# Optimization experiments

Hardware: AMD Instinct MI355X
Metric: run time of the kernel (lower is better)

The kernel has to match this reference:

```python
import jax, jax.numpy as jnp
import numpy as np

N = 50000      # nodes
E = 800000     # edges (before self loops)
IN_DIM = 256
HID = 64       # per-head hidden dim
HEADS = 4
NEG_SLOPE = 0.2


def setup_inputs() -> dict:
    key = jax.random.key(0)
    k1, k2, k3, k4, k5, k6 = jax.random.split(key, 6)
    x = jax.random.normal(k1, (N, IN_DIM), dtype=jnp.float32)
    edge_index = jax.random.randint(k2, (2, E), 0, N, dtype=jnp.int64)
    # GATConv params (PyG layout): lin weight, att_src, att_dst, bias
    W = jax.random.normal(k3, (IN_DIM, HEADS * HID), dtype=jnp.float32) / np.sqrt(IN_DIM)
    att_src = jax.random.normal(k4, (HEADS, HID), dtype=jnp.float32) / np.sqrt(HID)
    att_dst = jax.random.normal(k5, (HEADS, HID), dtype=jnp.float32) / np.sqrt(HID)
    bias = jnp.zeros((HEADS * HID,), dtype=jnp.float32)
    return {"x": x, "edge_index": edge_index, "W": W,
            "att_src": att_src, "att_dst": att_dst, "bias": bias}


def _gat_forward(x, edge_index, W, att_src, att_dst, bias):
    n = x.shape[0]
    # linear projection per head: [N, H, F]
    h = (x @ W).reshape(n, HEADS, HID)
    # per-node attention logits (computed once on nodes, then gathered)
    a_src = jnp.einsum('nhf,hf->nh', h, att_src)  # [N, H]
    a_dst = jnp.einsum('nhf,hf->nh', h, att_dst)  # [N, H]
    # add self loops (PyG default add_self_loops=True)
    loop = jnp.arange(n, dtype=edge_index.dtype)
    src = jnp.concatenate([edge_index[0], loop])  # [E+N]
    dst = jnp.concatenate([edge_index[1], loop])  # [E+N]
    # edge attention logits with LeakyReLU
    e = jax.nn.leaky_relu(a_src[src] + a_dst[dst], NEG_SLOPE)  # [E+N, H]
    # segment softmax over incoming edges of each destination node
    m = jax.ops.segment_max(e, dst, num_segments=n)            # [N, H]
    num = jnp.exp(e - m[dst])                                  # [E+N, H]
    denom = jax.ops.segment_sum(num, dst, num_segments=n)      # [N, H]
    alpha = num / denom[dst]                                   # [E+N, H]
    # scatter-aggregate weighted source features
    msg = alpha[:, :, None] * h[src]                           # [E+N, H, F]
    out = jax.ops.segment_sum(msg, dst, num_segments=n)        # [N, H, F]
    out = out.reshape(n, HEADS * HID) + bias
    # GraphEncoder.forward: ReLU then Dropout (dropout=0 -> identity)
    return jax.nn.relu(out)


def reference(x, edge_index, W, att_src, att_dst, bias):
    return _gat_forward(x, edge_index, W, att_src, att_dst, bias)
```

## Files before the change

### kernel.cpp

```cpp
#include <hip/hip_runtime.h>
#include <hip/hip_bf16.h>

#define N_NODES 50000
#define N_EDGES 800000
#define TOT_EDGES (N_EDGES + N_NODES)
#define IN_DIM 256
#define OUT_DIM 256
#define HEADS 4
#define NEG_SLOPE 0.2f
#define MAXD 128

#define GBLK 782
#define HBLK 512
#define LDS_STRIDE 264

typedef __bf16 bf16x8 __attribute__((ext_vector_type(8)));
typedef __bf16 bf16x4 __attribute__((ext_vector_type(4)));
typedef float f32x4 __attribute__((ext_vector_type(4)));

__device__ __forceinline__ float b2f(unsigned short u) {
    union { float f; unsigned int i; } v; v.i = ((unsigned int)u) << 16; return v.f;
}

__device__ __forceinline__ bool detect64(const int* __restrict__ ei, int t) {
    int nz = 0;
    for (int i = t; i < 1024; i += 256)
        if (ei[2 * i + 1] != 0) nz++;
    return __syncthreads_count(nz) == 0;
}

struct Args {
    const float* x; const int* ei; const float* W;
    const float* att_s; const float* att_d; const float* bias;
    float* out;
    __bf16* Wt; __bf16* h; float* a_src; float* a_dst;
    int* counts; int* loc; int* bsum; int* bpref;
    int* offsets; int* cursor; int* csr_src;
};

__global__ void k_wt(Args A) {
    int k = blockIdx.x;
    int n = threadIdx.x;
    A.Wt[(size_t)n * IN_DIM + k] = (__bf16)A.W[(size_t)k * OUT_DIM + n];
}

__global__ __launch_bounds__(256) void k_gemm_hist(Args A) {
    __shared__ __bf16 xs[64 * LDS_STRIDE];
    const int t = threadIdx.x;

    if (blockIdx.x < GBLK) {
        const int mbase = blockIdx.x * 64;
        const float4* x4 = (const float4*)A.x;
#pragma unroll
        for (int i = 0; i < 16; ++i) {
            int f = i * 256 + t;
            int row = f >> 6;
            int c4  = f & 63;
            int grow = mbase + row;
            if (grow >= N_NODES) grow = N_NODES - 1;
            float4 v = x4[(size_t)grow * 64 + c4];
            bf16x4 o = { (__bf16)v.x, (__bf16)v.y, (__bf16)v.z, (__bf16)v.w };
            *(bf16x4*)&xs[row * LDS_STRIDE + c4 * 4] = o;
        }
        __syncthreads();

        const int wave = t >> 6;
        const int lane = t & 63;
        const int cc   = lane & 15;
        const int quad = lane >> 4;
        const int n0   = wave * 64;
        f32x4 acc[4][4];
#pragma unroll
        for (int mt = 0; mt < 4; ++mt)
#pragma unroll
            for (int j = 0; j < 4; ++j) acc[mt][j] = (f32x4){0.f, 0.f, 0.f, 0.f};

        for (int k0 = 0; k0 < IN_DIM; k0 += 32) {
            bf16x8 b0 = *(const bf16x8*)(A.Wt + (size_t)(n0 + cc)      * IN_DIM + k0 + quad * 8);
            bf16x8 b1 = *(const bf16x8*)(A.Wt + (size_t)(n0 + 16 + cc) * IN_DIM + k0 + quad * 8);
            bf16x8 b2 = *(const bf16x8*)(A.Wt + (size_t)(n0 + 32 + cc) * IN_DIM + k0 + quad * 8);
            bf16x8 b3 = *(const bf16x8*)(A.Wt + (size_t)(n0 + 48 + cc) * IN_DIM + k0 + quad * 8);
#pragma unroll
            for (int mt = 0; mt < 4; ++mt) {
                bf16x8 a = *(const bf16x8*)&xs[(mt * 16 + cc) * LDS_STRIDE + k0 + quad * 8];
                acc[mt][0] = __builtin_amdgcn_mfma_f32_16x16x32_bf16(a, b0, acc[mt][0], 0, 0, 0);
                acc[mt][1] = __builtin_amdgcn_mfma_f32_16x16x32_bf16(a, b1, acc[mt][1], 0, 0, 0);
                acc[mt][2] = __builtin_amdgcn_mfma_f32_16x16x32_bf16(a, b2, acc[mt][2], 0, 0, 0);
                acc[mt][3] = __builtin_amdgcn_mfma_f32_16x16x32_bf16(a, b3, acc[mt][3], 0, 0, 0);
            }
        }

        float as0 = A.att_s[n0 + cc],      as1 = A.att_s[n0 + 16 + cc];
        float as2 = A.att_s[n0 + 32 + cc], as3 = A.att_s[n0 + 48 + cc];
        float ad0 = A.att_d[n0 + cc],      ad1 = A.att_d[n0 + 16 + cc];
        float ad2 = A.att_d[n0 + 32 + cc], ad3 = A.att_d[n0 + 48 + cc];
#pragma unroll
        for (int mt = 0; mt < 4; ++mt) {
#pragma unroll
            for (int r = 0; r < 4; ++r) {
                int row = mbase + mt * 16 + quad * 4 + r;
                bool ok = row < N_NODES;
                float pS = acc[mt][0][r] * as0 + acc[mt][1][r] * as1
                         + acc[mt][2][r] * as2 + acc[mt][3][r] * as3;
                float pD = acc[mt][0][r] * ad0 + acc[mt][1][r] * ad1
                         + acc[mt][2][r] * ad2 + acc[mt][3][r] * ad3;
#pragma unroll
                for (int o = 8; o >= 1; o >>= 1) {
                    pS += __shfl_xor(pS, o, 64);
                    pD += __shfl_xor(pD, o, 64);
                }
                if (ok) {
                    __bf16* orow = A.h + (size_t)row * OUT_DIM + n0 + cc;
                    orow[0]  = (__bf16)acc[mt][0][r];
                    orow[16] = (__bf16)acc[mt][1][r];
                    orow[32] = (__bf16)acc[mt][2][r];
                    orow[48] = (__bf16)acc[mt][3][r];
                    if (cc == 0) {
                        A.a_src[row * 4 + wave] = pS;
                        A.a_dst[row * 4 + wave] = pD;
                    }
                }
            }
        }
    } else {
        bool is64 = detect64(A.ei, t);
        const long long* ei64 = (const long long*)A.ei;
        int bi = blockIdx.x - GBLK;
        for (int i = bi * 256 + t; i < N_EDGES; i += HBLK * 256) {
            int v = is64 ? (int)ei64[N_EDGES + i] : A.ei[N_EDGES + i];
            atomicAdd(&A.counts[v], 1);
        }
    }
}

#define SBLK 1024
#define NBLK ((N_NODES + SBLK - 1) / SBLK)
__global__ __launch_bounds__(1024) void k_scanA(Args A) {
    __shared__ int s[SBLK];
    int t = threadIdx.x, idx = blockIdx.x * SBLK + t;
    int cval = (idx < N_NODES) ? A.counts[idx] + 1 : 0;
    s[t] = cval;
    __syncthreads();
    for (int off = 1; off < SBLK; off <<= 1) {
        int v = (t >= off) ? s[t - off] : 0;
        __syncthreads();
        s[t] += v;
        __syncthreads();
    }
    if (idx < N_NODES) A.loc[idx] = s[t] - cval;
    if (t == SBLK - 1) A.bsum[blockIdx.x] = s[t];
}

__global__ void k_scanB(Args A) {
    int lane = threadIdx.x;
    int v = (lane < NBLK) ? A.bsum[lane] : 0;
    int orig = v;
#pragma unroll
    for (int off = 1; off < 64; off <<= 1) {
        int u = __shfl_up(v, off, 64);
        if (lane >= off) v += u;
    }
    if (lane < NBLK) A.bpref[lane] = v - orig;
    if (lane == 0) A.offsets[N_NODES] = TOT_EDGES;
}

__global__ void k_scanC(Args A) {
    int idx = blockIdx.x * blockDim.x + threadIdx.x;
    if (idx < N_NODES) {
        int o = A.loc[idx] + A.bpref[idx >> 10];
        A.offsets[idx] = o;
        A.cursor[idx] = o;
    }
}

__global__ __launch_bounds__(256) void k_fill(Args A) {
    bool is64 = detect64(A.ei, threadIdx.x);
    int i = blockIdx.x * blockDim.x + threadIdx.x;
    const long long* ei64 = (const long long*)A.ei;
    if (i < N_EDGES) {
        int s, d;
        if (is64) { s = (int)ei64[i]; d = (int)ei64[N_EDGES + i]; }
        else      { s = A.ei[i];      d = A.ei[N_EDGES + i]; }
        int pos = atomicAdd(&A.cursor[d], 1);
        A.csr_src[pos] = s;
    } else if (i < TOT_EDGES) {
        int n = i - N_EDGES;
        int pos = atomicAdd(&A.cursor[n], 1);
        A.csr_src[pos] = n;
    }
}

__global__ __launch_bounds__(256) void k_agg(Args A) {
    __shared__ float lds_all[4][MAXD][4];
    int wave = threadIdx.x >> 6, lane = threadIdx.x & 63;
    int node = blockIdx.x * 4 + wave;
    if (node >= N_NODES) return;
    float (*lds)[4] = lds_all[wave];

    int base = A.offsets[node];
    int deg  = A.offsets[node + 1] - base;
    const float4* as4 = (const float4*)A.a_src;
    float4 ad = ((const float4*)A.a_dst)[node];

    float4 smv = {0.f, 0.f, 0.f, 0.f};
    for (int e = lane; e < deg; e += 64) {
        int s = A.csr_src[base + e];
        float4 av = as4[s];
        float4 l;
        l.x = av.x + ad.x; l.x = l.x > 0.f ? l.x : NEG_SLOPE * l.x;
        l.y = av.y + ad.y; l.y = l.y > 0.f ? l.y : NEG_SLOPE * l.y;
        l.z = av.z + ad.z; l.z = l.z > 0.f ? l.z : NEG_SLOPE * l.z;
        l.w = av.w + ad.w; l.w = l.w > 0.f ? l.w : NEG_SLOPE * l.w;
        float4 e4;
        e4.x = __expf(l.x); e4.y = __expf(l.y);
        e4.z = __expf(l.z); e4.w = __expf(l.w);
        smv.x += e4.x; smv.y += e4.y; smv.z += e4.z; smv.w += e4.w;
        if (e < MAXD) { lds[e][0] = e4.x; lds[e][1] = e4.y; lds[e][2] = e4.z; lds[e][3] = e4.w; }
    }
    int padEnd = (deg + 3) & ~3;
    if (padEnd > MAXD) padEnd = MAXD;
    for (int e = deg + lane; e < padEnd; e += 64) {
        lds[e][0] = 0.f; lds[e][1] = 0.f; lds[e][2] = 0.f; lds[e][3] = 0.f;
    }
#pragma unroll
    for (int o = 32; o >= 1; o >>= 1) {
        smv.x += __shfl_xor(smv.x, o, 64);
        smv.y += __shfl_xor(smv.y, o, 64);
        smv.z += __shfl_xor(smv.z, o, 64);
        smv.w += __shfl_xor(smv.w, o, 64);
    }

    int head = lane >> 4;
    float smh = head == 0 ? smv.x : head == 1 ? smv.y : head == 2 ? smv.z : smv.w;
    float adh = head == 0 ? ad.x  : head == 1 ? ad.y  : head == 2 ? ad.z  : ad.w;
    float inv_d = 1.f / smh;

    float acc0 = 0.f, acc1 = 0.f, acc2 = 0.f, acc3 = 0.f;
    const unsigned short* hs = reinterpret_cast<const unsigned short*>(A.h);
    int degc = deg < MAXD ? deg : MAXD;
    int rEnd = (degc + 3) & ~3;
    for (int e = 0; e < rEnd; e += 4) {
        int s0 = A.csr_src[base + e];
        int s1 = A.csr_src[base + ((e + 1 < deg) ? e + 1 : 0)];
        int s2 = A.csr_src[base + ((e + 2 < deg) ? e + 2 : 0)];
        int s3 = A.csr_src[base + ((e + 3 < deg) ? e + 3 : 0)];
        float al0 = lds[e][head];
        float al1 = lds[e + 1][head];
        float al2 = lds[e + 2][head];
        float al3 = lds[e + 3][head];
        ushort4 h0 = *(const ushort4*)(hs + (size_t)s0 * OUT_DIM + lane * 4);
        ushort4 h1 = *(const ushort4*)(hs + (size_t)s1 * OUT_DIM + lane * 4);
        ushort4 h2 = *(const ushort4*)(hs + (size_t)s2 * OUT_DIM + lane * 4);
        ushort4 h3 = *(const ushort4*)(hs + (size_t)s3 * OUT_DIM + lane * 4);
        acc0 += al0 * b2f(h0.x) + al1 * b2f(h1.x) + al2 * b2f(h2.x) + al3 * b2f(h3.x);
        acc1 += al0 * b2f(h0.y) + al1 * b2f(h1.y) + al2 * b2f(h2.y) + al3 * b2f(h3.y);
        acc2 += al0 * b2f(h0.z) + al1 * b2f(h1.z) + al2 * b2f(h2.z) + al3 * b2f(h3.z);
        acc3 += al0 * b2f(h0.w) + al1 * b2f(h1.w) + al2 * b2f(h2.w) + al3 * b2f(h3.w);
    }
    for (int e = MAXD; e < deg; ++e) {
        int s = A.csr_src[base + e];
        float a = A.a_src[s * 4 + head] + adh;
        a = a > 0.f ? a : NEG_SLOPE * a;
        float al = __expf(a);
        ushort4 hv = *(const ushort4*)(hs + (size_t)s * OUT_DIM + lane * 4);
        acc0 += al * b2f(hv.x); acc1 += al * b2f(hv.y);
        acc2 += al * b2f(hv.z); acc3 += al * b2f(hv.w);
    }

    float4 bv = ((const float4*)A.bias)[lane];
    float v0 = acc0 * inv_d + bv.x;
    float v1 = acc1 * inv_d + bv.y;
    float v2 = acc2 * inv_d + bv.z;
    float v3 = acc3 * inv_d + bv.w;
    float4 o4;
    o4.x = v0 > 0.f ? v0 : 0.f;
    o4.y = v1 > 0.f ? v1 : 0.f;
    o4.z = v2 > 0.f ? v2 : 0.f;
    o4.w = v3 > 0.f ? v3 : 0.f;
    ((float4*)A.out)[(size_t)node * 64 + lane] = o4;
}

extern "C" void kernel_launch(void* const* d_in, const int* in_sizes, int n_in,
                              void* d_out, int out_size, void* d_ws, size_t ws_size,
                              hipStream_t stream) {
    (void)out_size; (void)ws_size;
    const void* p_x = nullptr; const void* p_ei = nullptr; const void* p_W = nullptr;
    const void* p_small[3] = {nullptr, nullptr, nullptr}; int nsmall = 0;
    for (int i = 0; i < n_in; ++i) {
        switch (in_sizes[i]) {
            case N_NODES * IN_DIM:      p_x = d_in[i]; break;
            case 2 * N_EDGES:           p_ei = d_in[i]; break;
            case IN_DIM * OUT_DIM:      p_W = d_in[i]; break;
            case OUT_DIM:               if (nsmall < 3) p_small[nsmall++] = d_in[i]; break;
            default: break;
        }
    }
    if (!p_x)  p_x  = d_in[0];
    if (!p_ei) p_ei = d_in[1];
    if (!p_W)  p_W  = d_in[2];
    if (nsmall < 3) { p_small[0] = d_in[3]; p_small[1] = d_in[4]; p_small[2] = d_in[5]; }

    char* ws = (char*)d_ws;
    size_t off = 0;
    auto alloc = [&](size_t bytes) -> void* {
        void* p = ws + off;
        off = (off + bytes + 255) & ~(size_t)255;
        return p;
    };
    Args A;
    A.Wt      = (__bf16*)alloc((size_t)IN_DIM * OUT_DIM * 2);
    A.h       = (__bf16*)alloc((size_t)N_NODES * OUT_DIM * 2);
    A.a_src   = (float*)alloc((size_t)N_NODES * HEADS * 4);
    A.a_dst   = (float*)alloc((size_t)N_NODES * HEADS * 4);
    A.counts  = (int*)alloc((size_t)N_NODES * 4);
    A.loc     = (int*)alloc((size_t)N_NODES * 4);
    A.bsum    = (int*)alloc(NBLK * 4);
    A.bpref   = (int*)alloc(NBLK * 4);
    A.offsets = (int*)alloc((size_t)(N_NODES + 1) * 4);
    A.cursor  = (int*)alloc((size_t)N_NODES * 4);
    A.csr_src = (int*)alloc((size_t)TOT_EDGES * 4);

    A.x     = (const float*)p_x;
    A.ei    = (const int*)p_ei;
    A.W     = (const float*)p_W;
    A.att_s = (const float*)p_small[0];
    A.att_d = (const float*)p_small[1];
    A.bias  = (const float*)p_small[2];
    A.out   = (float*)d_out;

    hipMemsetAsync(A.counts, 0, (size_t)N_NODES * 4, stream);
    k_wt<<<dim3(IN_DIM), dim3(OUT_DIM), 0, stream>>>(A);
    k_gemm_hist<<<dim3(GBLK + HBLK), dim3(256), 0, stream>>>(A);
    k_scanA<<<dim3(NBLK), dim3(SBLK), 0, stream>>>(A);
    k_scanB<<<dim3(1), dim3(64), 0, stream>>>(A);
    k_scanC<<<dim3((N_NODES + 255) / 256), dim3(256), 0, stream>>>(A);
    k_fill<<<dim3((TOT_EDGES + 255) / 256), dim3(256), 0, stream>>>(A);
    k_agg<<<dim3((N_NODES + 3) / 4), dim3(256), 0, stream>>>(A);
}
```

Before: 289.9 us.

## Restructure preprocessing pipeline: fuse scans, overlap CSR fill with GEMM

The weight transpose and the destination histogram now share one front kernel. The three scan kernels become one kernel that uses a last-block ticket to finish the block prefix and write offsets. The CSR fill now runs in spare blocks alongside the GEMM instead of after it. W is stored in a k-blocked bf16 layout so each B-fragment load reads contiguous 32-element chunks. The goal is fewer launches and less serialization, at the cost of relying on the ticket/threadfence protocol and having the fill atomics compete with the GEMM for the GPU.

```diff
diff --git a/kernel.cpp b/kernel.cpp
--- a/kernel.cpp
+++ b/kernel.cpp
@@ -11,7 +11,7 @@
 #define MAXD 128
 
 #define GBLK 782
-#define HBLK 512
+#define FBLK 512
 #define LDS_STRIDE 264
 
 typedef __bf16 bf16x8 __attribute__((ext_vector_type(8)));
@@ -33,18 +33,72 @@
     const float* x; const int* ei; const float* W;
     const float* att_s; const float* att_d; const float* bias;
     float* out;
-    __bf16* Wt; __bf16* h; float* a_src; float* a_dst;
+    __bf16* Wt;
+    __bf16* h; float* a_src; float* a_dst;
     int* counts; int* loc; int* bsum; int* bpref;
-    int* offsets; int* cursor; int* csr_src;
+    int* offsets; int* cursor; int* csr_src; int* ticket;
 };
 
-__global__ void k_wt(Args A) {
-    int k = blockIdx.x;
-    int n = threadIdx.x;
-    A.Wt[(size_t)n * IN_DIM + k] = (__bf16)A.W[(size_t)k * OUT_DIM + n];
-}
-
-__global__ __launch_bounds__(256) void k_gemm_hist(Args A) {
+__global__ __launch_bounds__(256) void k_front(Args A) {
+    if (blockIdx.x == 0 && threadIdx.x == 0) *A.ticket = 0;
+    bool is64 = detect64(A.ei, threadIdx.x);
+    int gid = blockIdx.x * 256 + threadIdx.x;
+    int gsz = gridDim.x * 256;
+    for (int i = gid; i < IN_DIM * OUT_DIM; i += gsz) {
+        int n = i & 255, k = i >> 8;
+        A.Wt[((size_t)(k >> 5) * 256 + n) * 32 + (k & 31)] = (__bf16)A.W[(size_t)k * OUT_DIM + n];
+    }
+    const long long* ei64 = (const long long*)A.ei;
+    for (int i = gid; i < N_EDGES; i += gsz) {
+        int v = is64 ? (int)ei64[N_EDGES + i] : A.ei[N_EDGES + i];
+        atomicAdd(&A.counts[v], 1);
+    }
+}
+
+#define SBLK 1024
+#define NBLK ((N_NODES + SBLK - 1) / SBLK)
+__global__ __launch_bounds__(1024) void k_scan_all(Args A) {
+    __shared__ int s[SBLK];
+    __shared__ int bp[64];
+    __shared__ int lastflag;
+    int t = threadIdx.x, idx = blockIdx.x * SBLK + t;
+    int cval = (idx < N_NODES) ? A.counts[idx] + 1 : 0;
+    s[t] = cval;
+    __syncthreads();
+    for (int off = 1; off < SBLK; off <<= 1) {
+        int v = (t >= off) ? s[t - off] : 0;
+        __syncthreads();
+        s[t] += v;
+        __syncthreads();
+    }
+    if (idx < N_NODES) A.loc[idx] = s[t] - cval;
+    if (t == SBLK - 1) A.bsum[blockIdx.x] = s[t];
+    __threadfence();
+    __syncthreads();
+    if (t == 0) lastflag = (atomicAdd(A.ticket, 1) == NBLK - 1) ? 1 : 0;
+    __syncthreads();
+    if (!lastflag) return;
+    __threadfence();
+    if (t < 64) {
+        int v = (t < NBLK) ? A.bsum[t] : 0;
+        int orig = v;
+#pragma unroll
+        for (int off = 1; off < 64; off <<= 1) {
+            int u = __shfl_up(v, off, 64);
+            if (t >= off) v += u;
+        }
+        bp[t] = v - orig;
+        if (t == 0) A.offsets[N_NODES] = TOT_EDGES;
+    }
+    __syncthreads();
+    for (int i = t; i < N_NODES; i += SBLK) {
+        int o = A.loc[i] + bp[i >> 10];
+        A.offsets[i] = o;
+        A.cursor[i] = o;
+    }
+}
+
+__global__ __launch_bounds__(256) void k_gemm_fill(Args A) {
     __shared__ __bf16 xs[64 * LDS_STRIDE];
     const int t = threadIdx.x;
 
@@ -76,10 +130,11 @@
             for (int j = 0; j < 4; ++j) acc[mt][j] = (f32x4){0.f, 0.f, 0.f, 0.f};
 
         for (int k0 = 0; k0 < IN_DIM; k0 += 32) {
-            bf16x8 b0 = *(const bf16x8*)(A.Wt + (size_t)(n0 + cc)      * IN_DIM + k0 + quad * 8);
-            bf16x8 b1 = *(const bf16x8*)(A.Wt + (size_t)(n0 + 16 + cc) * IN_DIM + k0 + quad * 8);
-            bf16x8 b2 = *(const bf16x8*)(A.Wt + (size_t)(n0 + 32 + cc) * IN_DIM + k0 + quad * 8);
-            bf16x8 b3 = *(const bf16x8*)(A.Wt + (size_t)(n0 + 48 + cc) * IN_DIM + k0 + quad * 8);
+            const __bf16* wb = A.Wt + ((size_t)(k0 >> 5) * 256) * 32 + quad * 8;
+            bf16x8 b0 = *(const bf16x8*)(wb + (size_t)(n0 + cc)      * 32);
+            bf16x8 b1 = *(const bf16x8*)(wb + (size_t)(n0 + 16 + cc) * 32);
+            bf16x8 b2 = *(const bf16x8*)(wb + (size_t)(n0 + 32 + cc) * 32);
+            bf16x8 b3 = *(const bf16x8*)(wb + (size_t)(n0 + 48 + cc) * 32);
 #pragma unroll
             for (int mt = 0; mt < 4; ++mt) {
                 bf16x8 a = *(const bf16x8*)&xs[(mt * 16 + cc) * LDS_STRIDE + k0 + quad * 8];
@@ -126,67 +181,19 @@
         bool is64 = detect64(A.ei, t);
         const long long* ei64 = (const long long*)A.ei;
         int bi = blockIdx.x - GBLK;
-        for (int i = bi * 256 + t; i < N_EDGES; i += HBLK * 256) {
-            int v = is64 ? (int)ei64[N_EDGES + i] : A.ei[N_EDGES + i];
-            atomicAdd(&A.counts[v], 1);
-        }
-    }
-}
-
-#define SBLK 1024
-#define NBLK ((N_NODES + SBLK - 1) / SBLK)
-__global__ __launch_bounds__(1024) void k_scanA(Args A) {
-    __shared__ int s[SBLK];
-    int t = threadIdx.x, idx = blockIdx.x * SBLK + t;
-    int cval = (idx < N_NODES) ? A.counts[idx] + 1 : 0;
-    s[t] = cval;
-    __syncthreads();
-    for (int off = 1; off < SBLK; off <<= 1) {
-        int v = (t >= off) ? s[t - off] : 0;
-        __syncthreads();
-        s[t] += v;
-        __syncthreads();
-    }
-    if (idx < N_NODES) A.loc[idx] = s[t] - cval;
-    if (t == SBLK - 1) A.bsum[blockIdx.x] = s[t];
-}
-
-__global__ void k_scanB(Args A) {
-    int lane = threadIdx.x;
-    int v = (lane < NBLK) ? A.bsum[lane] : 0;
-    int orig = v;
-#pragma unroll
-    for (int off = 1; off < 64; off <<= 1) {
-        int u = __shfl_up(v, off, 64);
-        if (lane >= off) v += u;
-    }
-    if (lane < NBLK) A.bpref[lane] = v - orig;
-    if (lane == 0) A.offsets[N_NODES] = TOT_EDGES;
-}
-
-__global__ void k_scanC(Args A) {
-    int idx = blockIdx.x * blockDim.x + threadIdx.x;
-    if (idx < N_NODES) {
-        int o = A.loc[idx] + A.bpref[idx >> 10];
-        A.offsets[idx] = o;
-        A.cursor[idx] = o;
-    }
-}
-
-__global__ __launch_bounds__(256) void k_fill(Args A) {
-    bool is64 = detect64(A.ei, threadIdx.x);
-    int i = blockIdx.x * blockDim.x + threadIdx.x;
-    const long long* ei64 = (const long long*)A.ei;
-    if (i < N_EDGES) {
-        int s, d;
-        if (is64) { s = (int)ei64[i]; d = (int)ei64[N_EDGES + i]; }
-        else      { s = A.ei[i];      d = A.ei[N_EDGES + i]; }
-        int pos = atomicAdd(&A.cursor[d], 1);
-        A.csr_src[pos] = s;
-    } else if (i < TOT_EDGES) {
-        int n = i - N_EDGES;
-        int pos = atomicAdd(&A.cursor[n], 1);
-        A.csr_src[pos] = n;
+        for (int i = bi * 256 + t; i < TOT_EDGES; i += FBLK * 256) {
+            if (i < N_EDGES) {
+                int s, d;
+                if (is64) { s = (int)ei64[i]; d = (int)ei64[N_EDGES + i]; }
+                else      { s = A.ei[i];      d = A.ei[N_EDGES + i]; }
+                int pos = atomicAdd(&A.cursor[d], 1);
+                A.csr_src[pos] = s;
+            } else {
+                int n = i - N_EDGES;
+                int pos = atomicAdd(&A.cursor[n], 1);
+                A.csr_src[pos] = n;
+            }
+        }
     }
 }
 
@@ -319,6 +326,7 @@
     A.offsets = (int*)alloc((size_t)(N_NODES + 1) * 4);
     A.cursor  = (int*)alloc((size_t)N_NODES * 4);
     A.csr_src = (int*)alloc((size_t)TOT_EDGES * 4);
+    A.ticket  = (int*)alloc(4);
 
     A.x     = (const float*)p_x;
     A.ei    = (const int*)p_ei;
@@ -329,11 +337,8 @@
     A.out   = (float*)d_out;
 
     hipMemsetAsync(A.counts, 0, (size_t)N_NODES * 4, stream);
-    k_wt<<<dim3(IN_DIM), dim3(OUT_DIM), 0, stream>>>(A);
-    k_gemm_hist<<<dim3(GBLK + HBLK), dim3(256), 0, stream>>>(A);
-    k_scanA<<<dim3(NBLK), dim3(SBLK), 0, stream>>>(A);
-    k_scanB<<<dim3(1), dim3(64), 0, stream>>>(A);
-    k_scanC<<<dim3((N_NODES + 255) / 256), dim3(256), 0, stream>>>(A);
-    k_fill<<<dim3((TOT_EDGES + 255) / 256), dim3(256), 0, stream>>>(A);
+    k_front<<<dim3(1024), dim3(256), 0, stream>>>(A);
+    k_scan_all<<<dim3(NBLK), dim3(SBLK), 0, stream>>>(A);
+    k_gemm_fill<<<dim3(GBLK + FBLK), dim3(256), 0, stream>>>(A);
     k_agg<<<dim3((N_NODES + 3) / 4), dim3(256), 0, stream>>>(A);
 }
```

Measured after the change: 292.1 us. About the same (+0.8%).
